# Optimization experiments

Measured on AMD Instinct MI355X. Metric: run time of the kernel, lower is better.

## Reference

```python
import jax, jax.numpy as jnp
import numpy as np

EMBED_DIM = 1024
NUM_HEADS = 16
HEAD_DIM = EMBED_DIM // NUM_HEADS


def setup_inputs() -> dict:
    key = jax.random.key(0)
    ks = jax.random.split(key, 11)
    B, N, C = 2, 2048, EMBED_DIM
    s = 1.0 / np.sqrt(C)
    return {
        "query": jax.random.normal(ks[0], (B, N, C), jnp.float32),
        "key": jax.random.normal(ks[1], (B, N, C), jnp.float32),
        "value": jax.random.normal(ks[2], (B, N, C), jnp.float32),
        # torch nn.Linear weights: [out_features, in_features]
        "Wq": jax.random.normal(ks[3], (C, C), jnp.float32) * s,
        "bq": jnp.zeros((C,), jnp.float32),
        "Wk": jax.random.normal(ks[4], (C, C), jnp.float32) * s,
        "bk": jnp.zeros((C,), jnp.float32),
        "Wv": jax.random.normal(ks[5], (C, C), jnp.float32) * s,
        "bv": jnp.zeros((C,), jnp.float32),
        "Wo": jax.random.normal(ks[6], (C, C), jnp.float32) * s,
        "bo": jnp.zeros((C,), jnp.float32),
    }


def reference(query, key, value, Wq, bq, Wk, bk, Wv, bv, Wo, bo):
    B, N, C = query.shape
    H, D = NUM_HEADS, HEAD_DIM
    # projections (torch Linear: x @ W.T + b)
    q = query @ Wq.T + bq
    k = key @ Wk.T + bk
    v = value @ Wv.T + bv
    # [B, N, C] -> [B, H, N, D]
    q = q.reshape(B, N, H, D).transpose(0, 2, 1, 3)
    k = k.reshape(B, N, H, D).transpose(0, 2, 1, 3)
    v = v.reshape(B, N, H, D).transpose(0, 2, 1, 3)
    # scores: [B, H, N, N]
    scores = jnp.einsum("bhqd,bhkd->bhqk", q, k) / jnp.sqrt(jnp.asarray(D, q.dtype))
    attn = jax.nn.softmax(scores, axis=-1)
    # attend: [B, H, N, D] -> [B, N, C]
    out = jnp.einsum("bhqk,bhkd->bhqd", attn, v)
    out = out.transpose(0, 2, 1, 3).reshape(B, N, C)
    return out @ Wo.T + bo
```

## Files before the change

kernel.cpp:

```cpp
#include <hip/hip_runtime.h>
#include <hip/hip_bf16.h>
#include <cstdint>

typedef short bf16x8 __attribute__((ext_vector_type(8)));
typedef float f32x4 __attribute__((ext_vector_type(4)));
typedef float f32x16 __attribute__((ext_vector_type(16)));
typedef uint32_t u32x4v __attribute__((ext_vector_type(4)));
typedef unsigned short u16;

#define BATCH 2
#define NTOK 2048
#define CDIM 1024
#define NHEAD 16
#define DHEAD 64
#define MROWS 4096
#define KDIM 1024
#define KVB 64
#define NT (NTOK / KVB)

__device__ __forceinline__ u16 f2bf(float x) {
    uint32_t b = __float_as_uint(x);
    uint32_t r = (b + 0x7fffu + ((b >> 16) & 1u)) >> 16;
    return (u16)r;
}

__device__ __forceinline__ uint32_t packbf2(float lo, float hi) {
    float2 f; f.x = lo; f.y = hi;
    __hip_bfloat162 h = __float22bfloat162_rn(f);
    uint32_t r;
    __builtin_memcpy(&r, &h, 4);
    return r;
}

__device__ __forceinline__ void gload_lds16(const void* g, void* l) {
    __builtin_amdgcn_global_load_lds((const __attribute__((address_space(1))) void*)g,
                                     (__attribute__((address_space(3))) void*)l,
                                     16, 0, 0);
}

__global__ __launch_bounds__(256) void cast_kernel(
    const float* __restrict__ q, const float* __restrict__ k, const float* __restrict__ v,
    const float* __restrict__ wq, const float* __restrict__ wk, const float* __restrict__ wv,
    const float* __restrict__ wo, u16* __restrict__ dst) {
    const size_t TOT = 16u << 20;
    size_t i0 = ((size_t)blockIdx.x * 256 + threadIdx.x) * 4;
    size_t stride = (size_t)gridDim.x * 256 * 4;
    for (size_t i = i0; i < TOT; i += stride) {
        const float* src;
        size_t off = i;
        if (i < (4u << 20))        { src = q;  }
        else if (i < (8u << 20))   { src = k;  off = i - (4u << 20); }
        else if (i < (12u << 20))  { src = v;  off = i - (8u << 20); }
        else if (i < (13u << 20))  { src = wq; off = i - (12u << 20); }
        else if (i < (14u << 20))  { src = wk; off = i - (13u << 20); }
        else if (i < (15u << 20))  { src = wv; off = i - (14u << 20); }
        else                       { src = wo; off = i - (15u << 20); }
        float4 f = *(const float4*)(src + off);
        u16 o0 = f2bf(f.x), o1 = f2bf(f.y), o2 = f2bf(f.z), o3 = f2bf(f.w);
        uint2 packed;
        packed.x = (uint32_t)o0 | ((uint32_t)o1 << 16);
        packed.y = (uint32_t)o2 | ((uint32_t)o3 << 16);
        *(uint2*)(dst + i) = packed;
    }
}

__global__ __launch_bounds__(256, 3) void gemm_qkv(
    const u16* __restrict__ Xq, const u16* __restrict__ Xk, const u16* __restrict__ Xv,
    const u16* __restrict__ Wq, const u16* __restrict__ Wk, const u16* __restrict__ Wv,
    const float* __restrict__ bq, const float* __restrict__ bk, const float* __restrict__ bv,
    u16* __restrict__ Qo, u16* __restrict__ Ko, u16* __restrict__ Vo) {
    __shared__ u16 sA[128 * 32];
    __shared__ u16 sB[128 * 32];
    const int tid = threadIdx.x;
    const int lane = tid & 63;
    const int wave = tid >> 6;
    const int z = blockIdx.z;
    const u16* A  = (z == 0) ? Xq : (z == 1) ? Xk : Xv;
    const u16* Bw = (z == 0) ? Wq : (z == 1) ? Wk : Wv;
    const float* bias = (z == 0) ? bq : (z == 1) ? bk : bv;
    u16* Out = (z == 0) ? Qo : (z == 1) ? Ko : Vo;
    const float scale = (z == 0) ? 0.125f * 1.44269504088896f : 1.0f;

    const int m0 = blockIdx.x * 128, n0 = blockIdx.y * 128;
    const int wm = (wave >> 1) * 64, wn = (wave & 1) * 64;
    f32x4 acc[4][4] = {};
    const int rsel = lane & 15;
    const int ksel = (lane >> 4) * 8;

    for (int k0 = 0; k0 < KDIM; k0 += 32) {
#pragma unroll
        for (int u = 0; u < 2; ++u) {
            int c = tid + u * 256;
            int row = c >> 2, cin = c & 3;
            gload_lds16(A + (size_t)(m0 + row) * KDIM + k0 + cin * 8, &sA[c * 8]);
            gload_lds16(Bw + (size_t)(n0 + row) * KDIM + k0 + cin * 8, &sB[c * 8]);
        }
        __syncthreads();
        bf16x8 af[4], bfr[4];
#pragma unroll
        for (int i = 0; i < 4; ++i)
            af[i] = *(const bf16x8*)&sA[(wm + i * 16 + rsel) * 32 + ksel];
#pragma unroll
        for (int j = 0; j < 4; ++j)
            bfr[j] = *(const bf16x8*)&sB[(wn + j * 16 + rsel) * 32 + ksel];
#pragma unroll
        for (int i = 0; i < 4; ++i)
#pragma unroll
            for (int j = 0; j < 4; ++j)
                acc[i][j] = __builtin_amdgcn_mfma_f32_16x16x32_bf16(af[i], bfr[j], acc[i][j], 0, 0, 0);
        __syncthreads();
    }

#pragma unroll
    for (int i = 0; i < 4; ++i) {
        int mbase = m0 + wm + i * 16 + (lane >> 4) * 4;
#pragma unroll
        for (int j = 0; j < 4; ++j) {
            int n = n0 + wn + j * 16 + (lane & 15);
            float bv2 = bias[n];
            int h = n >> 6, d = n & 63;
#pragma unroll
            for (int r = 0; r < 4; ++r) {
                int m = mbase + r;
                int b = m >> 11, tok = m & 2047;
                Out[(((size_t)(b * NHEAD + h)) * NTOK + tok) * DHEAD + d] =
                    f2bf((acc[i][j][r] + bv2) * scale);
            }
        }
    }
}

__global__ __launch_bounds__(256, 3) void gemm_out(
    const u16* __restrict__ A,
    const u16* __restrict__ Bw,
    const float* __restrict__ bias,
    float* __restrict__ Out,
    int M, int N, int K) {
    __shared__ u16 sA[128 * 32];
    __shared__ u16 sB[128 * 32];
    const int tid = threadIdx.x;
    const int lane = tid & 63;
    const int wave = tid >> 6;
    const int m0 = blockIdx.x * 128, n0 = blockIdx.y * 128;
    const int wm = (wave >> 1) * 64, wn = (wave & 1) * 64;
    f32x4 acc[4][4] = {};
    const int rsel = lane & 15;
    const int ksel = (lane >> 4) * 8;

    for (int k0 = 0; k0 < K; k0 += 32) {
#pragma unroll
        for (int u = 0; u < 2; ++u) {
            int c = tid + u * 256;
            int row = c >> 2, cin = c & 3;
            gload_lds16(A + (size_t)(m0 + row) * K + k0 + cin * 8, &sA[c * 8]);
            gload_lds16(Bw + (size_t)(n0 + row) * K + k0 + cin * 8, &sB[c * 8]);
        }
        __syncthreads();
        bf16x8 af[4], bfr[4];
#pragma unroll
        for (int i = 0; i < 4; ++i)
            af[i] = *(const bf16x8*)&sA[(wm + i * 16 + rsel) * 32 + ksel];
#pragma unroll
        for (int j = 0; j < 4; ++j)
            bfr[j] = *(const bf16x8*)&sB[(wn + j * 16 + rsel) * 32 + ksel];
#pragma unroll
        for (int i = 0; i < 4; ++i)
#pragma unroll
            for (int j = 0; j < 4; ++j)
                acc[i][j] = __builtin_amdgcn_mfma_f32_16x16x32_bf16(af[i], bfr[j], acc[i][j], 0, 0, 0);
        __syncthreads();
    }

#pragma unroll
    for (int i = 0; i < 4; ++i) {
        int mbase = m0 + wm + i * 16 + (lane >> 4) * 4;
#pragma unroll
        for (int j = 0; j < 4; ++j) {
            int n = n0 + wn + j * 16 + (lane & 15);
            float bv = bias[n];
#pragma unroll
            for (int r = 0; r < 4; ++r) {
                int m = mbase + r;
                Out[(size_t)m * N + n] = acc[i][j][r] + bv;
            }
        }
    }
}

__global__ __launch_bounds__(256, 2) void attn_kernel(
    const u16* __restrict__ Qg, const u16* __restrict__ Kg, const u16* __restrict__ Vg,
    u16* __restrict__ Og) {
    __shared__ u16 Ks[2][KVB * 64];
    __shared__ uint32_t Vt[2][64 * 32];
    const int tid = threadIdx.x, lane = tid & 63, wave = tid >> 6;
    const int hi = lane >> 5, lq = lane & 31;

    int flat = blockIdx.x;
    int vflat = (flat & 7) * 64 + (flat >> 3);
    int bh = vflat >> 4;
    int qtile = vflat & 15;

    const int h = bh & (NHEAD - 1), b = bh >> 4;
    const u16* Qh = Qg + (size_t)bh * NTOK * DHEAD;
    const u16* Kh = Kg + (size_t)bh * NTOK * DHEAD;
    const u16* Vh = Vg + (size_t)bh * NTOK * DHEAD;
    const int qrow0 = qtile * 128 + wave * 32;
    const int qr = qrow0 + lq;

    bf16x8 qf[4];
#pragma unroll
    for (int dk = 0; dk < 4; ++dk)
        qf[dk] = *(const bf16x8*)&Qh[(size_t)qr * DHEAD + dk * 16 + hi * 8];

    f32x16 acc0 = {}, acc1 = {};
    float mrun = -1e30f, lrun = 0.f;

    const int pr = ((lq >> 2) & 1) * 8 + (lq & 3) + ((lq >> 3) & 1) * 4 + (lq >> 4) * 16;

    const int jp = tid & 31, od = tid >> 5;

    {
        const u16* vp = Vh + (size_t)(2 * jp) * DHEAD + od * 8;
        uint4 pva = *(const uint4*)vp;
        uint4 pvb = *(const uint4*)(vp + DHEAD);
#pragma unroll
        for (int u = 0; u < 2; ++u) {
            int c2 = tid + u * 256;
            int kv = c2 >> 3, gi = c2 & 7;
            gload_lds16(Kh + (size_t)kv * DHEAD + (gi ^ (kv & 7)) * 8, &Ks[0][c2 * 8]);
        }
        uint32_t aw[4] = {pva.x, pva.y, pva.z, pva.w};
        uint32_t bw[4] = {pvb.x, pvb.y, pvb.z, pvb.w};
        char* vn = (char*)&Vt[0][0];
#pragma unroll
        for (int i = 0; i < 8; ++i) {
            int d = od * 8 + i;
            uint32_t lo = (aw[i >> 1] >> ((i & 1) * 16)) & 0xffffu;
            uint32_t hi16 = (bw[i >> 1] >> ((i & 1) * 16)) & 0xffffu;
            *(uint32_t*)(vn + d * 128 + ((jp * 4) ^ ((d & 7) << 4))) = lo | (hi16 << 16);
        }
    }
    __syncthreads();

    int cur = 0;
    for (int t = 0; t < NT; ++t) {
        const bool pre = (t + 1 < NT);
        uint4 wva, wvb;
        if (pre) {
            const u16* vp = Vh + (size_t)((t + 1) * KVB + 2 * jp) * DHEAD + od * 8;
            wva = *(const uint4*)vp;
            wvb = *(const uint4*)(vp + DHEAD);
#pragma unroll
            for (int u = 0; u < 2; ++u) {
                int c2 = tid + u * 256;
                int kv = c2 >> 3, gi = c2 & 7;
                gload_lds16(Kh + (size_t)((t + 1) * KVB + kv) * DHEAD + (gi ^ (kv & 7)) * 8,
                            &Ks[cur ^ 1][c2 * 8]);
            }
        }

        f32x16 T0 = {}, T1 = {};
        const char* kb_ = (const char*)&Ks[cur][0];
        __builtin_amdgcn_s_setprio(1);
#pragma unroll
        for (int dk = 0; dk < 4; ++dk) {
            int x = dk * 32 + hi * 16;
            int kv0 = pr, kv1 = 32 + pr;
            bf16x8 k0 = *(const bf16x8*)(kb_ + kv0 * 128 + (x ^ ((kv0 & 7) << 4)));
            bf16x8 k1 = *(const bf16x8*)(kb_ + kv1 * 128 + (x ^ ((kv1 & 7) << 4)));
            T0 = __builtin_amdgcn_mfma_f32_32x32x16_bf16(k0, qf[dk], T0, 0, 0, 0);
            T1 = __builtin_amdgcn_mfma_f32_32x32x16_bf16(k1, qf[dk], T1, 0, 0, 0);
        }
        __builtin_amdgcn_s_setprio(0);

        float m16[16];
#pragma unroll
        for (int i = 0; i < 16; ++i) m16[i] = fmaxf(T0[i], T1[i]);
#pragma unroll
        for (int s2 = 8; s2 >= 1; s2 >>= 1)
#pragma unroll
            for (int i = 0; i < s2; ++i) m16[i] = fmaxf(m16[i], m16[i + s2]);
        float mx = fmaxf(m16[0], __shfl_xor(m16[0], 32));

        if (mx > mrun + 11.0f) {
            float scl = __builtin_amdgcn_exp2f(mrun - mx);
            mrun = mx;
            lrun *= scl;
            acc0 *= scl;
            acc1 *= scl;
        }

        float p0[16], p1[16];
#pragma unroll
        for (int i = 0; i < 16; ++i) {
            p0[i] = __builtin_amdgcn_exp2f(T0[i] - mrun);
            p1[i] = __builtin_amdgcn_exp2f(T1[i] - mrun);
        }
        float sm[16];
#pragma unroll
        for (int i = 0; i < 16; ++i) sm[i] = p0[i] + p1[i];
#pragma unroll
        for (int s2 = 8; s2 >= 1; s2 >>= 1)
#pragma unroll
            for (int i = 0; i < s2; ++i) sm[i] += sm[i + s2];
        lrun += sm[0] + __shfl_xor(sm[0], 32);

        bf16x8 pf[4];
#pragma unroll
        for (int kb2 = 0; kb2 < 2; ++kb2) {
            const float* pp = kb2 ? p1 : p0;
#pragma unroll
            for (int hh = 0; hh < 2; ++hh) {
                int rb = hh * 8;
                u32x4v w = { packbf2(pp[rb + 0], pp[rb + 1]),
                             packbf2(pp[rb + 2], pp[rb + 3]),
                             packbf2(pp[rb + 4], pp[rb + 5]),
                             packbf2(pp[rb + 6], pp[rb + 7]) };
                pf[kb2 * 2 + hh] = *(bf16x8*)&w;
            }
        }

        const char* vb_ = (const char*)&Vt[cur][0];
        __builtin_amdgcn_s_setprio(1);
#pragma unroll
        for (int db = 0; db < 2; ++db) {
            int d = db * 32 + lq;
#pragma unroll
            for (int ks = 0; ks < 4; ++ks) {
                int off = d * 128 + ((ks * 32 + hi * 16) ^ ((d & 7) << 4));
                bf16x8 vf = *(const bf16x8*)(vb_ + off);
                if (db == 0)
                    acc0 = __builtin_amdgcn_mfma_f32_32x32x16_bf16(vf, pf[ks], acc0, 0, 0, 0);
                else
                    acc1 = __builtin_amdgcn_mfma_f32_32x32x16_bf16(vf, pf[ks], acc1, 0, 0, 0);
            }
        }
        __builtin_amdgcn_s_setprio(0);

        if (pre) {
            uint32_t aw[4] = {wva.x, wva.y, wva.z, wva.w};
            uint32_t bw[4] = {wvb.x, wvb.y, wvb.z, wvb.w};
            char* vn = (char*)&Vt[cur ^ 1][0];
#pragma unroll
            for (int i = 0; i < 8; ++i) {
                int d = od * 8 + i;
                uint32_t lo = (aw[i >> 1] >> ((i & 1) * 16)) & 0xffffu;
                uint32_t hi16 = (bw[i >> 1] >> ((i & 1) * 16)) & 0xffffu;
                *(uint32_t*)(vn + d * 128 + ((jp * 4) ^ ((d & 7) << 4))) = lo | (hi16 << 16);
            }
        }
        __syncthreads();
        cur ^= 1;
    }

    float rinv = 1.0f / lrun;
#pragma unroll
    for (int db = 0; db < 2; ++db) {
#pragma unroll
        for (int rq = 0; rq < 4; ++rq) {
            int based = db * 32 + 8 * rq + 4 * hi;
            float o0, o1, o2, o3;
            if (db == 0) {
                o0 = acc0[rq * 4 + 0]; o1 = acc0[rq * 4 + 1];
                o2 = acc0[rq * 4 + 2]; o3 = acc0[rq * 4 + 3];
            } else {
                o0 = acc1[rq * 4 + 0]; o1 = acc1[rq * 4 + 1];
                o2 = acc1[rq * 4 + 2]; o3 = acc1[rq * 4 + 3];
            }
            uint2 st;
            st.x = packbf2(o0 * rinv, o1 * rinv);
            st.y = packbf2(o2 * rinv, o3 * rinv);
            *(uint2*)&Og[((size_t)(b * NTOK + qr)) * CDIM + h * DHEAD + based] = st;
        }
    }
}

extern "C" void kernel_launch(void* const* d_in, const int* in_sizes, int n_in,
                              void* d_out, int out_size, void* d_ws, size_t ws_size,
                              hipStream_t stream) {
    const float* q  = (const float*)d_in[0];
    const float* k  = (const float*)d_in[1];
    const float* v  = (const float*)d_in[2];
    const float* Wq = (const float*)d_in[3];
    const float* bq = (const float*)d_in[4];
    const float* Wk = (const float*)d_in[5];
    const float* bk = (const float*)d_in[6];
    const float* Wv = (const float*)d_in[7];
    const float* bv = (const float*)d_in[8];
    const float* Wo = (const float*)d_in[9];
    const float* bo = (const float*)d_in[10];

    u16* wsp = (u16*)d_ws;
    u16* Xq  = wsp;
    u16* Xk  = Xq + (4u << 20);
    u16* Xv  = Xk + (4u << 20);
    u16* Wqb = Xv + (4u << 20);
    u16* Wkb = Wqb + (1u << 20);
    u16* Wvb = Wkb + (1u << 20);
    u16* Wob = Wvb + (1u << 20);
    u16* Qb  = Wob + (1u << 20);
    u16* Kb  = Qb + (4u << 20);
    u16* Vb  = Kb + (4u << 20);
    u16* Ab  = Xq;

    cast_kernel<<<2048, 256, 0, stream>>>(q, k, v, Wq, Wk, Wv, Wo, Xq);

    gemm_qkv<<<dim3(MROWS / 128, CDIM / 128, 3), 256, 0, stream>>>(
        Xq, Xk, Xv, Wqb, Wkb, Wvb, bq, bk, bv, Qb, Kb, Vb);

    attn_kernel<<<512, 256, 0, stream>>>(Qb, Kb, Vb, Ab);

    gemm_out<<<dim3(MROWS / 128, CDIM / 128), 256, 0, stream>>>(
        Ab, Wob, bo, (float*)d_out, MROWS, CDIM, KDIM);
}
```

Before: 137.8 us.

## Write V transposed from projection GEMM and async-load it into attention LDS

The QKV projection epilogue now stores the V output in a [b,h,d,tok] transposed layout using packed bf16x4 stores. The attention kernel then loads V tiles straight into LDS with async global-to-LDS copies, using the same XOR swizzle as K, and drops the register-staged in-kernel transpose. The row-sum reduction is moved after the PV MFMAs so it can overlap with them. This removes per-tile VALU pack work and LDS scatter stores, at the cost of a strided V store pattern in the projection epilogue. It also assumes the V LDS layout matches what the unchanged PV read code expects.

Result: faster. 133.9 us (-2.9%).

```diff
diff --git a/kernel.cpp b/kernel.cpp
--- a/kernel.cpp
+++ b/kernel.cpp
@@ -111,20 +111,38 @@
         __syncthreads();
     }
 
-#pragma unroll
-    for (int i = 0; i < 4; ++i) {
-        int mbase = m0 + wm + i * 16 + (lane >> 4) * 4;
-#pragma unroll
-        for (int j = 0; j < 4; ++j) {
-            int n = n0 + wn + j * 16 + (lane & 15);
-            float bv2 = bias[n];
-            int h = n >> 6, d = n & 63;
-#pragma unroll
-            for (int r = 0; r < 4; ++r) {
-                int m = mbase + r;
-                int b = m >> 11, tok = m & 2047;
-                Out[(((size_t)(b * NHEAD + h)) * NTOK + tok) * DHEAD + d] =
-                    f2bf((acc[i][j][r] + bv2) * scale);
+    if (z != 2) {
+#pragma unroll
+        for (int i = 0; i < 4; ++i) {
+            int mbase = m0 + wm + i * 16 + (lane >> 4) * 4;
+#pragma unroll
+            for (int j = 0; j < 4; ++j) {
+                int n = n0 + wn + j * 16 + (lane & 15);
+                float bv2 = bias[n];
+                int h = n >> 6, d = n & 63;
+#pragma unroll
+                for (int r = 0; r < 4; ++r) {
+                    int m = mbase + r;
+                    int b = m >> 11, tok = m & 2047;
+                    Out[(((size_t)(b * NHEAD + h)) * NTOK + tok) * DHEAD + d] =
+                        f2bf((acc[i][j][r] + bv2) * scale);
+                }
+            }
+        }
+    } else {
+#pragma unroll
+        for (int i = 0; i < 4; ++i) {
+            int mbase = m0 + wm + i * 16 + (lane >> 4) * 4;
+            int b = mbase >> 11, tok = mbase & 2047;
+#pragma unroll
+            for (int j = 0; j < 4; ++j) {
+                int n = n0 + wn + j * 16 + (lane & 15);
+                float bv2 = bias[n];
+                int h = n >> 6, d = n & 63;
+                uint2 st;
+                st.x = packbf2(acc[i][j][0] + bv2, acc[i][j][1] + bv2);
+                st.y = packbf2(acc[i][j][2] + bv2, acc[i][j][3] + bv2);
+                *(uint2*)&Out[(((size_t)(b * NHEAD + h)) * DHEAD + d) * NTOK + tok] = st;
             }
         }
     }
@@ -191,7 +209,7 @@
     const u16* __restrict__ Qg, const u16* __restrict__ Kg, const u16* __restrict__ Vg,
     u16* __restrict__ Og) {
     __shared__ u16 Ks[2][KVB * 64];
-    __shared__ uint32_t Vt[2][64 * 32];
+    __shared__ u16 Vt[2][64 * KVB];
     const int tid = threadIdx.x, lane = tid & 63, wave = tid >> 6;
     const int hi = lane >> 5, lq = lane & 31;
 
@@ -203,7 +221,7 @@
     const int h = bh & (NHEAD - 1), b = bh >> 4;
     const u16* Qh = Qg + (size_t)bh * NTOK * DHEAD;
     const u16* Kh = Kg + (size_t)bh * NTOK * DHEAD;
-    const u16* Vh = Vg + (size_t)bh * NTOK * DHEAD;
+    const u16* VhT = Vg + (size_t)bh * DHEAD * NTOK;
     const int qrow0 = qtile * 128 + wave * 32;
     const int qr = qrow0 + lq;
 
@@ -217,27 +235,18 @@
 
     const int pr = ((lq >> 2) & 1) * 8 + (lq & 3) + ((lq >> 3) & 1) * 4 + (lq >> 4) * 16;
 
-    const int jp = tid & 31, od = tid >> 5;
-
     {
-        const u16* vp = Vh + (size_t)(2 * jp) * DHEAD + od * 8;
-        uint4 pva = *(const uint4*)vp;
-        uint4 pvb = *(const uint4*)(vp + DHEAD);
 #pragma unroll
         for (int u = 0; u < 2; ++u) {
             int c2 = tid + u * 256;
             int kv = c2 >> 3, gi = c2 & 7;
             gload_lds16(Kh + (size_t)kv * DHEAD + (gi ^ (kv & 7)) * 8, &Ks[0][c2 * 8]);
         }
-        uint32_t aw[4] = {pva.x, pva.y, pva.z, pva.w};
-        uint32_t bw[4] = {pvb.x, pvb.y, pvb.z, pvb.w};
-        char* vn = (char*)&Vt[0][0];
-#pragma unroll
-        for (int i = 0; i < 8; ++i) {
-            int d = od * 8 + i;
-            uint32_t lo = (aw[i >> 1] >> ((i & 1) * 16)) & 0xffffu;
-            uint32_t hi16 = (bw[i >> 1] >> ((i & 1) * 16)) & 0xffffu;
-            *(uint32_t*)(vn + d * 128 + ((jp * 4) ^ ((d & 7) << 4))) = lo | (hi16 << 16);
+#pragma unroll
+        for (int u = 0; u < 2; ++u) {
+            int c2 = tid + u * 256;
+            int d = c2 >> 3, gi = c2 & 7;
+            gload_lds16(VhT + (size_t)d * NTOK + (gi ^ (d & 7)) * 8, &Vt[0][c2 * 8]);
         }
     }
     __syncthreads();
@@ -245,17 +254,20 @@
     int cur = 0;
     for (int t = 0; t < NT; ++t) {
         const bool pre = (t + 1 < NT);
-        uint4 wva, wvb;
         if (pre) {
-            const u16* vp = Vh + (size_t)((t + 1) * KVB + 2 * jp) * DHEAD + od * 8;
-            wva = *(const uint4*)vp;
-            wvb = *(const uint4*)(vp + DHEAD);
 #pragma unroll
             for (int u = 0; u < 2; ++u) {
                 int c2 = tid + u * 256;
                 int kv = c2 >> 3, gi = c2 & 7;
                 gload_lds16(Kh + (size_t)((t + 1) * KVB + kv) * DHEAD + (gi ^ (kv & 7)) * 8,
                             &Ks[cur ^ 1][c2 * 8]);
+            }
+#pragma unroll
+            for (int u = 0; u < 2; ++u) {
+                int c2 = tid + u * 256;
+                int d = c2 >> 3, gi = c2 & 7;
+                gload_lds16(VhT + (size_t)d * NTOK + (t + 1) * KVB + (gi ^ (d & 7)) * 8,
+                            &Vt[cur ^ 1][c2 * 8]);
             }
         }
 
@@ -296,14 +308,6 @@
             p0[i] = __builtin_amdgcn_exp2f(T0[i] - mrun);
             p1[i] = __builtin_amdgcn_exp2f(T1[i] - mrun);
         }
-        float sm[16];
-#pragma unroll
-        for (int i = 0; i < 16; ++i) sm[i] = p0[i] + p1[i];
-#pragma unroll
-        for (int s2 = 8; s2 >= 1; s2 >>= 1)
-#pragma unroll
-            for (int i = 0; i < s2; ++i) sm[i] += sm[i + s2];
-        lrun += sm[0] + __shfl_xor(sm[0], 32);
 
         bf16x8 pf[4];
 #pragma unroll
@@ -337,18 +341,15 @@
         }
         __builtin_amdgcn_s_setprio(0);
 
-        if (pre) {
-            uint32_t aw[4] = {wva.x, wva.y, wva.z, wva.w};
-            uint32_t bw[4] = {wvb.x, wvb.y, wvb.z, wvb.w};
-            char* vn = (char*)&Vt[cur ^ 1][0];
-#pragma unroll
-            for (int i = 0; i < 8; ++i) {
-                int d = od * 8 + i;
-                uint32_t lo = (aw[i >> 1] >> ((i & 1) * 16)) & 0xffffu;
-                uint32_t hi16 = (bw[i >> 1] >> ((i & 1) * 16)) & 0xffffu;
-                *(uint32_t*)(vn + d * 128 + ((jp * 4) ^ ((d & 7) << 4))) = lo | (hi16 << 16);
-            }
-        }
+        float sm[16];
+#pragma unroll
+        for (int i = 0; i < 16; ++i) sm[i] = p0[i] + p1[i];
+#pragma unroll
+        for (int s2 = 8; s2 >= 1; s2 >>= 1)
+#pragma unroll
+            for (int i = 0; i < s2; ++i) sm[i] += sm[i + s2];
+        lrun += sm[0] + __shfl_xor(sm[0], 32);
+
         __syncthreads();
         cur ^= 1;
     }
```
